# Optimization experiments

Measured on AMD Instinct MI355X. Metric: run time of the kernel, lower is better.

The kernel has to match this reference:

```python
import jax, jax.numpy as jnp
import numpy as np

NUM_FIELDS = 32
EMBED_DIM = 64
INTERACT_DIM = NUM_FIELDS * (NUM_FIELDS - 1) // 2  # 496


def setup_inputs() -> dict:
    key = jax.random.key(0)
    k1, k2 = jax.random.split(key)
    feature_emb = jax.random.normal(k1, (2048, NUM_FIELDS, EMBED_DIM), dtype=jnp.float32)
    # Xavier-normal init for bilinear_W: std = sqrt(2/(fan_in+fan_out)) = sqrt(2/(D+D))
    std = float(np.sqrt(2.0 / (EMBED_DIM + EMBED_DIM)))
    bilinear_W = jax.random.normal(k2, (INTERACT_DIM, EMBED_DIM, EMBED_DIM), dtype=jnp.float32) * std
    return {"feature_emb": feature_emb, "bilinear_W": bilinear_W}


def reference(feature_emb, bilinear_W):
    # field_interaction: for pair p = (i, j) (i < j, in itertools.combinations order),
    # out[:, p, :] = (v_i @ W_p) * v_j
    nf = feature_emb.shape[1]
    i_idx, j_idx = jnp.triu_indices(nf, k=1)  # matches combinations(range(nf), 2) order
    v_i = feature_emb[:, i_idx, :]  # [B, P, D]
    v_j = feature_emb[:, j_idx, :]  # [B, P, D]
    # batched tiny matmuls over all P pairs at once
    proj = jnp.einsum('bpd,pde->bpe', v_i, bilinear_W)  # [B, P, D]
    return proj * v_j  # [B, P, D] == concat over pairs along dim=1
```

## Files before the change

### kernel.cpp

```cpp
#include <hip/hip_runtime.h>
#include <hip/hip_bf16.h>

#define NB 2048
#define NF 32
#define ED 64
#define NP 496
#define BM 64

typedef __attribute__((ext_vector_type(8))) short short8;
typedef __attribute__((ext_vector_type(4))) float f32x4;

__device__ __forceinline__ unsigned short f2bf(float f) {
    unsigned int u = __builtin_bit_cast(unsigned int, f);
    u += 0x7fffu + ((u >> 16) & 1u);
    return (unsigned short)(u >> 16);
}

__device__ __forceinline__ unsigned long long pack4bf(float4 v) {
    return  (unsigned long long)f2bf(v.x)
         | ((unsigned long long)f2bf(v.y) << 16)
         | ((unsigned long long)f2bf(v.z) << 32)
         | ((unsigned long long)f2bf(v.w) << 48);
}

__global__ __launch_bounds__(256)
void bilinear_mfma_kernel(const float* __restrict__ emb,
                          const float* __restrict__ W,
                          float* __restrict__ out)
{
    const int bid  = blockIdx.x;
    const int p    = bid >> 5;
    const int bblk = bid & 31;
    const int b0   = bblk * BM;

    int fi = 0, rem = p;
    while (rem >= 31 - fi) { rem -= 31 - fi; ++fi; }
    const int fj = fi + 1 + rem;

    __shared__ unsigned short As[64][72];
    __shared__ unsigned short Ws[64][72];
    __shared__ float          Pr[64][68];

    const int tid = threadIdx.x;
    const int r   = tid >> 2;
    const int s   = tid & 3;

    {
        const float* src = emb + ((size_t)(b0 + r) * NF + fi) * ED;
        #pragma unroll
        for (int q = 0; q < 4; ++q) {
            const int e = q * 16 + s * 4;
            float4 v = *(const float4*)(src + e);
            *(unsigned long long*)&As[r][e] = pack4bf(v);
        }
    }

    {
        const float* wsrc = W + (size_t)p * (ED * ED) + r * ED;
        #pragma unroll
        for (int q = 0; q < 4; ++q) {
            const int e = q * 16 + s * 4;
            float4 v = *(const float4*)(wsrc + e);
            Ws[e + 0][r] = f2bf(v.x);
            Ws[e + 1][r] = f2bf(v.y);
            Ws[e + 2][r] = f2bf(v.z);
            Ws[e + 3][r] = f2bf(v.w);
        }
    }

    __syncthreads();

    const int wv   = tid >> 6;
    const int lane = tid & 63;
    const int lm   = lane & 15;
    const int h    = lane >> 4;
    const int m    = wv * 16 + lm;

    short8 a0 = *(const short8*)&As[m][h * 8];
    short8 a1 = *(const short8*)&As[m][32 + h * 8];

    f32x4 acc[4];
    #pragma unroll
    for (int nt = 0; nt < 4; ++nt) {
        acc[nt] = (f32x4){0.f, 0.f, 0.f, 0.f};
        short8 b0v = *(const short8*)&Ws[nt * 16 + lm][h * 8];
        short8 b1v = *(const short8*)&Ws[nt * 16 + lm][32 + h * 8];
        acc[nt] = __builtin_amdgcn_mfma_f32_16x16x32_bf16(a0, b0v, acc[nt], 0, 0, 0);
        acc[nt] = __builtin_amdgcn_mfma_f32_16x16x32_bf16(a1, b1v, acc[nt], 0, 0, 0);
    }

    const int row0 = wv * 16 + h * 4;
    #pragma unroll
    for (int nt = 0; nt < 4; ++nt) {
        #pragma unroll
        for (int rg = 0; rg < 4; ++rg)
            Pr[row0 + rg][nt * 16 + lm] = acc[nt][rg];
    }

    const float* vjp = emb + ((size_t)(b0 + r) * NF + fj) * ED;
    float*       op  = out + ((size_t)(b0 + r) * NP + p) * ED;
    #pragma unroll
    for (int q = 0; q < 4; ++q) {
        const int e = q * 16 + s * 4;
        float4 vj = *(const float4*)(vjp + e);
        float4 pr = *(const float4*)&Pr[r][e];
        float4 o;
        o.x = pr.x * vj.x;
        o.y = pr.y * vj.y;
        o.z = pr.z * vj.z;
        o.w = pr.w * vj.w;
        *(float4*)(op + e) = o;
    }
}

extern "C" void kernel_launch(void* const* d_in, const int* in_sizes, int n_in,
                              void* d_out, int out_size, void* d_ws, size_t ws_size,
                              hipStream_t stream) {
    const float* emb = (const float*)d_in[0];
    const float* W   = (const float*)d_in[1];
    float* out       = (float*)d_out;

    dim3 grid(NP * (NB / BM));
    dim3 block(256);
    bilinear_mfma_kernel<<<grid, block, 0, stream>>>(emb, W, out);
}
```

Measured before the change: 325.2 us.

## Precompute bf16 embeddings and transposed bf16 weights in workspace before main kernel

Two prep kernels convert the embeddings to bf16 and the bilinear weights to transposed bf16 in the workspace on every call. The main kernel then loads bf16 tiles with 16-byte vector copies instead of converting fp32 per block and doing scalar transposed LDS stores. This halves the repeated per-block reads of emb and W and removes the conflict-prone transpose writes. In exchange it adds two extra launches, and the v_j operand of the final multiply becomes bf16 instead of fp32, which slightly lowers accuracy. A fallback keeps the old path when the workspace is too small.

After: 290.5 us. 1.12x faster.

```diff
diff --git a/kernel.cpp b/kernel.cpp
--- a/kernel.cpp
+++ b/kernel.cpp
@@ -9,24 +9,64 @@
 
 typedef __attribute__((ext_vector_type(8))) short short8;
 typedef __attribute__((ext_vector_type(4))) float f32x4;
+typedef unsigned long long u64;
 
 __device__ __forceinline__ unsigned short f2bf(float f) {
     unsigned int u = __builtin_bit_cast(unsigned int, f);
     u += 0x7fffu + ((u >> 16) & 1u);
     return (unsigned short)(u >> 16);
 }
-
-__device__ __forceinline__ unsigned long long pack4bf(float4 v) {
-    return  (unsigned long long)f2bf(v.x)
-         | ((unsigned long long)f2bf(v.y) << 16)
-         | ((unsigned long long)f2bf(v.z) << 32)
-         | ((unsigned long long)f2bf(v.w) << 48);
-}
-
-__global__ __launch_bounds__(256)
-void bilinear_mfma_kernel(const float* __restrict__ emb,
-                          const float* __restrict__ W,
-                          float* __restrict__ out)
+__device__ __forceinline__ float bf2f(unsigned short h) {
+    unsigned int u = ((unsigned int)h) << 16;
+    return __builtin_bit_cast(float, u);
+}
+
+__global__ __launch_bounds__(256)
+void prep_wt(const float* __restrict__ W, unsigned short* __restrict__ Wt)
+{
+    __shared__ float Ls[64][65];
+    const int p = blockIdx.x, t = threadIdx.x;
+    const int r = t >> 2, s = t & 3;
+    const float* src = W + (size_t)p * 4096 + (size_t)r * 64;
+    #pragma unroll
+    for (int q = 0; q < 4; ++q) {
+        const int e = q * 16 + s * 4;
+        float4 v = *(const float4*)(src + e);
+        Ls[r][e + 0] = v.x; Ls[r][e + 1] = v.y;
+        Ls[r][e + 2] = v.z; Ls[r][e + 3] = v.w;
+    }
+    __syncthreads();
+    unsigned short* dst = Wt + (size_t)p * 4096 + (size_t)r * 64;
+    #pragma unroll
+    for (int q = 0; q < 4; ++q) {
+        const int d0 = q * 16 + s * 4;
+        u64 pk =  (u64)f2bf(Ls[d0 + 0][r])
+               | ((u64)f2bf(Ls[d0 + 1][r]) << 16)
+               | ((u64)f2bf(Ls[d0 + 2][r]) << 32)
+               | ((u64)f2bf(Ls[d0 + 3][r]) << 48);
+        *(u64*)(dst + d0) = pk;
+    }
+}
+
+__global__ __launch_bounds__(256)
+void prep_emb(const float* __restrict__ emb, unsigned short* __restrict__ Eb)
+{
+    const size_t g = (size_t)blockIdx.x * 256 + threadIdx.x;
+    const float* src = emb + g * 8;
+    float4 v0 = *(const float4*)src;
+    float4 v1 = *(const float4*)(src + 4);
+    short8 o;
+    o[0] = (short)f2bf(v0.x); o[1] = (short)f2bf(v0.y);
+    o[2] = (short)f2bf(v0.z); o[3] = (short)f2bf(v0.w);
+    o[4] = (short)f2bf(v1.x); o[5] = (short)f2bf(v1.y);
+    o[6] = (short)f2bf(v1.z); o[7] = (short)f2bf(v1.w);
+    *(short8*)(Eb + g * 8) = o;
+}
+
+__global__ __launch_bounds__(256)
+void bilinear_main(const unsigned short* __restrict__ Eb,
+                   const unsigned short* __restrict__ Wt,
+                   float* __restrict__ out)
 {
     const int bid  = blockIdx.x;
     const int p    = bid >> 5;
@@ -46,28 +86,15 @@
     const int s   = tid & 3;
 
     {
-        const float* src = emb + ((size_t)(b0 + r) * NF + fi) * ED;
-        #pragma unroll
-        for (int q = 0; q < 4; ++q) {
-            const int e = q * 16 + s * 4;
-            float4 v = *(const float4*)(src + e);
-            *(unsigned long long*)&As[r][e] = pack4bf(v);
-        }
-    }
-
-    {
-        const float* wsrc = W + (size_t)p * (ED * ED) + r * ED;
-        #pragma unroll
-        for (int q = 0; q < 4; ++q) {
-            const int e = q * 16 + s * 4;
-            float4 v = *(const float4*)(wsrc + e);
-            Ws[e + 0][r] = f2bf(v.x);
-            Ws[e + 1][r] = f2bf(v.y);
-            Ws[e + 2][r] = f2bf(v.z);
-            Ws[e + 3][r] = f2bf(v.w);
-        }
-    }
-
+        const unsigned short* src = Eb + ((size_t)(b0 + r) * NF + fi) * ED;
+        *(short8*)&As[r][s * 8]      = *(const short8*)(src + s * 8);
+        *(short8*)&As[r][32 + s * 8] = *(const short8*)(src + 32 + s * 8);
+    }
+    {
+        const unsigned short* src = Wt + (size_t)p * (ED * ED) + (size_t)r * ED;
+        *(short8*)&Ws[r][s * 8]      = *(const short8*)(src + s * 8);
+        *(short8*)&Ws[r][32 + s * 8] = *(const short8*)(src + 32 + s * 8);
+    }
     __syncthreads();
 
     const int wv   = tid >> 6;
@@ -97,18 +124,97 @@
             Pr[row0 + rg][nt * 16 + lm] = acc[nt][rg];
     }
 
+    const unsigned short* vjp = Eb + ((size_t)(b0 + r) * NF + fj) * ED;
+    float* op = out + ((size_t)(b0 + r) * NP + p) * ED;
+    #pragma unroll
+    for (int hb = 0; hb < 2; ++hb) {
+        const int e0 = hb * 32 + s * 8;
+        short8 vjv = *(const short8*)(vjp + e0);
+        float4 p0 = *(const float4*)&Pr[r][e0];
+        float4 p1 = *(const float4*)&Pr[r][e0 + 4];
+        float4 o0, o1;
+        o0.x = p0.x * bf2f((unsigned short)vjv[0]);
+        o0.y = p0.y * bf2f((unsigned short)vjv[1]);
+        o0.z = p0.z * bf2f((unsigned short)vjv[2]);
+        o0.w = p0.w * bf2f((unsigned short)vjv[3]);
+        o1.x = p1.x * bf2f((unsigned short)vjv[4]);
+        o1.y = p1.y * bf2f((unsigned short)vjv[5]);
+        o1.z = p1.z * bf2f((unsigned short)vjv[6]);
+        o1.w = p1.w * bf2f((unsigned short)vjv[7]);
+        *(float4*)(op + e0)     = o0;
+        *(float4*)(op + e0 + 4) = o1;
+    }
+}
+
+__global__ __launch_bounds__(256)
+void bilinear_fallback(const float* __restrict__ emb,
+                       const float* __restrict__ W,
+                       float* __restrict__ out)
+{
+    const int bid  = blockIdx.x;
+    const int p    = bid >> 5;
+    const int bblk = bid & 31;
+    const int b0   = bblk * BM;
+    int fi = 0, rem = p;
+    while (rem >= 31 - fi) { rem -= 31 - fi; ++fi; }
+    const int fj = fi + 1 + rem;
+
+    __shared__ unsigned short As[64][72];
+    __shared__ unsigned short Ws[64][72];
+    __shared__ float          Pr[64][68];
+
+    const int tid = threadIdx.x;
+    const int r   = tid >> 2;
+    const int s   = tid & 3;
+    {
+        const float* src = emb + ((size_t)(b0 + r) * NF + fi) * ED;
+        #pragma unroll
+        for (int q = 0; q < 4; ++q) {
+            const int e = q * 16 + s * 4;
+            float4 v = *(const float4*)(src + e);
+            u64 pk =  (u64)f2bf(v.x) | ((u64)f2bf(v.y) << 16)
+                   | ((u64)f2bf(v.z) << 32) | ((u64)f2bf(v.w) << 48);
+            *(u64*)&As[r][e] = pk;
+        }
+    }
+    {
+        const float* wsrc = W + (size_t)p * (ED * ED) + r * ED;
+        #pragma unroll
+        for (int q = 0; q < 4; ++q) {
+            const int e = q * 16 + s * 4;
+            float4 v = *(const float4*)(wsrc + e);
+            Ws[e + 0][r] = f2bf(v.x); Ws[e + 1][r] = f2bf(v.y);
+            Ws[e + 2][r] = f2bf(v.z); Ws[e + 3][r] = f2bf(v.w);
+        }
+    }
+    __syncthreads();
+    const int wv = tid >> 6, lane = tid & 63, lm = lane & 15, h = lane >> 4;
+    const int m = wv * 16 + lm;
+    short8 a0 = *(const short8*)&As[m][h * 8];
+    short8 a1 = *(const short8*)&As[m][32 + h * 8];
+    f32x4 acc[4];
+    #pragma unroll
+    for (int nt = 0; nt < 4; ++nt) {
+        acc[nt] = (f32x4){0.f, 0.f, 0.f, 0.f};
+        short8 b0v = *(const short8*)&Ws[nt * 16 + lm][h * 8];
+        short8 b1v = *(const short8*)&Ws[nt * 16 + lm][32 + h * 8];
+        acc[nt] = __builtin_amdgcn_mfma_f32_16x16x32_bf16(a0, b0v, acc[nt], 0, 0, 0);
+        acc[nt] = __builtin_amdgcn_mfma_f32_16x16x32_bf16(a1, b1v, acc[nt], 0, 0, 0);
+    }
+    const int row0 = wv * 16 + h * 4;
+    #pragma unroll
+    for (int nt = 0; nt < 4; ++nt)
+        #pragma unroll
+        for (int rg = 0; rg < 4; ++rg)
+            Pr[row0 + rg][nt * 16 + lm] = acc[nt][rg];
     const float* vjp = emb + ((size_t)(b0 + r) * NF + fj) * ED;
-    float*       op  = out + ((size_t)(b0 + r) * NP + p) * ED;
+    float* op = out + ((size_t)(b0 + r) * NP + p) * ED;
     #pragma unroll
     for (int q = 0; q < 4; ++q) {
         const int e = q * 16 + s * 4;
         float4 vj = *(const float4*)(vjp + e);
         float4 pr = *(const float4*)&Pr[r][e];
-        float4 o;
-        o.x = pr.x * vj.x;
-        o.y = pr.y * vj.y;
-        o.z = pr.z * vj.z;
-        o.w = pr.w * vj.w;
+        float4 o = { pr.x * vj.x, pr.y * vj.y, pr.z * vj.z, pr.w * vj.w };
         *(float4*)(op + e) = o;
     }
 }
@@ -120,7 +226,15 @@
     const float* W   = (const float*)d_in[1];
     float* out       = (float*)d_out;
 
-    dim3 grid(NP * (NB / BM));
-    dim3 block(256);
-    bilinear_mfma_kernel<<<grid, block, 0, stream>>>(emb, W, out);
-}
+    const size_t wt_bytes = (size_t)NP * ED * ED * 2;
+    const size_t eb_bytes = (size_t)NB * NF * ED * 2;
+    if (ws_size >= wt_bytes + eb_bytes) {
+        unsigned short* Wt = (unsigned short*)d_ws;
+        unsigned short* Eb = (unsigned short*)((char*)d_ws + wt_bytes);
+        prep_wt <<<NP, 256, 0, stream>>>(W, Wt);
+        prep_emb<<<(NB * NF * ED / 8) / 256, 256, 0, stream>>>(emb, Eb);
+        bilinear_main<<<NP * (NB / BM), 256, 0, stream>>>(Eb, Wt, out);
+    } else {
+        bilinear_fallback<<<NP * (NB / BM), 256, 0, stream>>>(emb, W, out);
+    }
+}
```
